# Kernel optimization log

Hardware: AMD Instinct MI355X
Metric: run time of the kernel (lower is better)

The kernel has to match this reference:

```python
import jax, jax.numpy as jnp
import numpy as np

DIM = 1024
H = 16
HD = DIM // H           # head_dim = 64
BS = 64                 # block_size
SPARSITY = 0.95
SCALE = HD ** -0.5


def setup_inputs() -> dict:
    key = jax.random.key(0)
    k1, k2, k3 = jax.random.split(key, 3)
    B, N = 2, 2048
    x = jax.random.normal(k1, (B, N, DIM), jnp.float32)
    # nn.Linear weights (out_features, in_features); qkv has no bias (qkv_bias=False)
    qkv_w = jax.random.normal(k2, (3 * DIM, DIM), jnp.float32) * (DIM ** -0.5)
    proj_w = jax.random.normal(k3, (DIM, DIM), jnp.float32) * (DIM ** -0.5)
    proj_b = jnp.zeros((DIM,), jnp.float32)
    return {"x": x, "qkv_w": qkv_w, "proj_w": proj_w, "proj_b": proj_b}


def reference(x, qkv_w, proj_w, proj_b):
    B, N, D = x.shape
    # qkv projection -> q,k,v each [B,H,N,HD]
    qkv = (x @ qkv_w.T).reshape(B, N, 3, H, HD).transpose(2, 0, 3, 1, 4)
    q, k, v = qkv[0], qkv[1], qkv[2]

    # --- CoarseCurvaturePredictor: block-level affinity + top-k block keep ---
    M = N // BS  # number of blocks (N divisible by block_size here)
    qb = q.reshape(B, H, M, BS, HD).mean(axis=3)  # [B,H,M,HD] coarse queries
    kb = k.reshape(B, H, M, BS, HD).mean(axis=3)  # [B,H,M,HD] coarse keys
    c = jnp.einsum('bhmd,bhnd->bhmn', qb, kb) * SCALE  # block scores [B,H,M,M]
    k_keep = max(1, int(round(M * (1.0 - SPARSITY))))  # blocks kept per row
    thresh = jax.lax.top_k(c, k_keep)[0][..., -1:]
    block_mask = (c >= thresh) | jnp.eye(M, dtype=bool)  # always keep diagonal

    # --- expand block mask to token level (repeat_interleave) ---
    tmask = jnp.repeat(jnp.repeat(block_mask, BS, axis=2), BS, axis=3)  # [B,H,N,N]

    # --- manual dense masked attention (faithful to fallback path) ---
    scores = jnp.einsum('bhqd,bhkd->bhqk', q, k) * SCALE
    scores = jnp.where(tmask, scores, -jnp.inf)
    probs = jax.nn.softmax(scores, axis=-1)
    out = jnp.einsum('bhqk,bhkd->bhqd', probs, v)
    out = out.transpose(0, 2, 1, 3).reshape(B, N, D)
    return out @ proj_w.T + proj_b
```

## Files before the change

kernel.cpp:

```cpp
#include <hip/hip_runtime.h>
#include <hip/hip_bf16.h>

#define BB 2
#define NN 2048
#define DIMD 1024
#define HH 16
#define HD64 64
#define MB 32
#define SCALE_F 0.125f

typedef __attribute__((ext_vector_type(8))) short bf16x8;
typedef __attribute__((ext_vector_type(8))) short short8v;
typedef __attribute__((ext_vector_type(4))) float f32x4;
typedef _Float16 f16;
typedef __attribute__((ext_vector_type(8))) _Float16 f16x8;
typedef __attribute__((ext_vector_type(4))) _Float16 f16x4;

#define VM_WAIT8 asm volatile("s_waitcnt vmcnt(8)" ::: "memory")
#define VM_WAIT6 asm volatile("s_waitcnt vmcnt(6)" ::: "memory")
#define VM_WAIT4 asm volatile("s_waitcnt vmcnt(4)" ::: "memory")
#define VM_WAIT0 asm volatile("s_waitcnt vmcnt(0)" ::: "memory")
#define SBAR __builtin_amdgcn_s_barrier()
#define SCHED0 __builtin_amdgcn_sched_barrier(0)

__device__ __forceinline__ unsigned short bf16_hi(float f) {
    return __builtin_bit_cast(unsigned short, __float2bfloat16(f));
}
__device__ __forceinline__ float bf16_val(unsigned short u) {
    return __bfloat162float(__builtin_bit_cast(__hip_bfloat16, u));
}
__device__ __forceinline__ short f16_bits(float f) {
    return __builtin_bit_cast(short, (f16)f);
}
__device__ __forceinline__ void async_copy16(const void* g, void* l) {
    __builtin_amdgcn_global_load_lds((const __attribute__((address_space(1))) void*)g,
                                     (__attribute__((address_space(3))) void*)l, 16, 0, 0);
}


__global__ __launch_bounds__(256) void split_in_fused_kernel(
    const float* __restrict__ x, short* __restrict__ Axs,
    const float* __restrict__ w, short* __restrict__ Wqs,
    const float* __restrict__ pw, short* __restrict__ Wp)
{
    const int bid = blockIdx.x;
    const float* src; short* dst; int idx;
    if (bid < 4096)      { src = x;  dst = Axs; idx = bid * 256 + threadIdx.x; }
    else if (bid < 7168) { src = w;  dst = Wqs; idx = (bid - 4096) * 256 + threadIdx.x; }
    else                 { src = pw; dst = Wp;  idx = (bid - 7168) * 256 + threadIdx.x; }
    int e = idx * 4;
    float4 v = *(const float4*)(src + e);
    ushort4 o = make_ushort4((unsigned short)f16_bits(v.x), (unsigned short)f16_bits(v.y),
                             (unsigned short)f16_bits(v.z), (unsigned short)f16_bits(v.w));
    *(ushort4*)(dst + e) = o;
}

__global__ __launch_bounds__(256) void qkv_mfma_kernel(
    const short* __restrict__ A, const short* __restrict__ W,
    short* __restrict__ QhI, short* __restrict__ KhI, short* __restrict__ VtI,
    float* __restrict__ qbf, float* __restrict__ kbf)
{
    __shared__ short SM[32768];
    const int wg = blockIdx.x;
    const int row0 = (wg / 24) * 128;
    const int col0 = (wg % 24) * 128;
    const int tid = threadIdx.x;
    const int lane = tid & 63;
    const int wave = tid >> 6;
    const int wm = wave & 1, wn = wave >> 1;

    auto AHS = [&](int b) { return SM + b * 8192; };
    auto WHS = [&](int b) { return SM + 16384 + b * 8192; };

    f32x4 acc[4][4];
    const f32x4 zero = {0.f, 0.f, 0.f, 0.f};
    #pragma unroll
    for (int i = 0; i < 4; ++i)
        #pragma unroll
        for (int j = 0; j < 4; ++j) acc[i][j] = zero;

    const int ldr = lane >> 2;
    const int lko = (((lane & 3) ^ ((lane >> 3) & 3))) * 8;
    const int rsl = ((lane >> 4) ^ ((lane >> 1) & 3)) * 8;

    auto stage = [&](int bufi, int ktn) {
        const int kk = ktn << 6;
        #pragma unroll
        for (int i = 0; i < 2; ++i) {
            const int chunk = wave * 2 + i;
            #pragma unroll
            for (int sub = 0; sub < 2; ++sub) {
                const short* gA = A + (size_t)(row0 + chunk * 16 + ldr) * 1024 + kk + sub * 32 + lko;
                const short* gW = W + (size_t)(col0 + chunk * 16 + ldr) * 1024 + kk + sub * 32 + lko;
                async_copy16(gA, (char*)AHS(bufi) + sub * 8192 + chunk * 1024);
                async_copy16(gW, (char*)WHS(bufi) + sub * 8192 + chunk * 1024);
            }
        }
    };

    auto compute = [&](int bufi) {
        #pragma unroll
        for (int sub = 0; sub < 2; ++sub) {
            const short* Ah = AHS(bufi) + sub * 4096;
            const short* Wh = WHS(bufi) + sub * 4096;
            f16x8 ah[4], wh[4];
            #pragma unroll
            for (int mi = 0; mi < 4; ++mi)
                ah[mi] = *(const f16x8*)(Ah + (wm * 64 + mi * 16 + (lane & 15)) * 32 + rsl);
            #pragma unroll
            for (int ni = 0; ni < 4; ++ni)
                wh[ni] = *(const f16x8*)(Wh + (wn * 64 + ni * 16 + (lane & 15)) * 32 + rsl);
            #pragma unroll
            for (int mi = 0; mi < 4; ++mi)
                #pragma unroll
                for (int ni = 0; ni < 4; ++ni)
                    acc[mi][ni] = __builtin_amdgcn_mfma_f32_16x16x32_f16(ah[mi], wh[ni], acc[mi][ni], 0, 0, 0);
        }
    };

    stage(0, 0);
    for (int kt = 0; kt < 14; kt += 2) {
        stage(1, kt + 1);
        VM_WAIT8; SBAR; SCHED0;
        compute(0);
        SBAR;
        stage(0, kt + 2);
        VM_WAIT8; SBAR; SCHED0;
        compute(1);
        SBAR;
    }
    stage(1, 15);
    VM_WAIT8; SBAR; SCHED0;
    compute(0);
    SBAR;
    VM_WAIT0; SBAR; SCHED0;
    compute(1);
    SBAR;

    const int gr_first = row0 + wm * 64;
    const int bb = gr_first >> 11;
    const int mblk = (gr_first & 2047) >> 6;
    const int gc0 = col0 + wn * 64;
    const int tsel = gc0 >> 10;
    const int h = (gc0 >> 6) & 15;
    const int tile = ((bb << 4) + h) * 32 + mblk;
    const float sc = (tsel == 0) ? SCALE_F : 1.0f;

    if (tsel != 2) {
        short* baseH = ((tsel == 0) ? QhI : KhI) + (size_t)tile * 4096;
        float* mdst  = ((tsel == 0) ? qbf : kbf) + ((size_t)((bb << 4) + h) * 32 + mblk) * 64;
        #pragma unroll
        for (int ni = 0; ni < 4; ++ni) {
            const int d = ni * 16 + (lane & 15);
            float colsum = 0.f;
            #pragma unroll
            for (int mi = 0; mi < 4; ++mi) {
                #pragma unroll
                for (int r = 0; r < 4; ++r) {
                    const int row = mi * 16 + (lane >> 4) * 4 + r;
                    float v = acc[mi][ni][r] * sc;
                    colsum += v;
                    const int off = (row * 64 + d) ^ ((row & 7) << 3);
                    baseH[off] = f16_bits(v);
                }
            }
            colsum += __shfl_xor(colsum, 16);
            colsum += __shfl_xor(colsum, 32);
            if ((lane >> 4) == 0) mdst[d] = colsum * (1.f / 64.f);
        }
    } else {
        short* tb = SM + wave * 4160;
        #pragma unroll
        for (int ni = 0; ni < 4; ++ni)
            #pragma unroll
            for (int mi = 0; mi < 4; ++mi)
                #pragma unroll
                for (int r = 0; r < 4; ++r) {
                    const int row = mi * 16 + (lane >> 4) * 4 + r;
                    const int d = ni * 16 + (lane & 15);
                    tb[row * 65 + d] = f16_bits(acc[mi][ni][r]);
                }
        short* vout = VtI + (size_t)tile * 4096;
        #pragma unroll
        for (int c = 0; c < 8; ++c) {
            short8v tv;
            #pragma unroll
            for (int j = 0; j < 8; ++j)
                tv[j] = tb[(c * 8 + j) * 65 + lane];
            const int off = (lane * 64 + c * 8) ^ ((lane & 7) << 3);
            *(short8v*)(vout + off) = tv;
        }
    }
}

__global__ __launch_bounds__(256) void scores_splitw_kernel(
    const float* __restrict__ qbf, const float* __restrict__ kbf,
    unsigned int* __restrict__ maskbits, float scale,
    const float* __restrict__ projw, short* __restrict__ Wdst)
{
    __shared__ float qs_[32][64];
    __shared__ float ks_[32][64];
    __shared__ float cb[32][32];
    const int bid = blockIdx.x;
    const int tid = threadIdx.x;

    if (bid >= 32) {
        int idx = (bid - 32) * 256 + tid;
        int e = idx * 4;
        float4 v = *(const float4*)(projw + e);
        ushort4 o = make_ushort4((unsigned short)f16_bits(v.x), (unsigned short)f16_bits(v.y),
                                 (unsigned short)f16_bits(v.z), (unsigned short)f16_bits(v.w));
        *(ushort4*)(Wdst + e) = o;
        return;
    }

    #pragma unroll
    for (int i = 0; i < 8; ++i) {
        int e = tid + i * 256;
        qs_[e >> 6][e & 63] = qbf[(size_t)bid * 2048 + e];
        ks_[e >> 6][e & 63] = kbf[(size_t)bid * 2048 + e];
    }
    __syncthreads();

    #pragma unroll
    for (int i = 0; i < 4; ++i) {
        int idx = tid + i * 256;
        int r = idx >> 5, c = idx & 31;
        float s = 0.f;
        #pragma unroll
        for (int d = 0; d < 64; ++d) s += qs_[r][d] * ks_[c][d];
        cb[r][c] = s * scale;
    }
    __syncthreads();

    if (tid < 32) {
        float m1 = -INFINITY, m2 = -INFINITY;
        for (int n = 0; n < 32; ++n) {
            float v = cb[tid][n];
            if (v > m1) { m2 = m1; m1 = v; }
            else if (v > m2) { m2 = v; }
        }
        unsigned int bits = 1u << tid;
        for (int n = 0; n < 32; ++n)
            if (cb[tid][n] >= m2) bits |= 1u << n;
        maskbits[bid * 32 + tid] = bits;
    }
}

__global__ __launch_bounds__(256) void proj_mfma_kernel(
    const short* __restrict__ A, const short* __restrict__ W,
    const float* __restrict__ bias, float* __restrict__ out)
{
    __shared__ short Ahs[2][8192];
    __shared__ short Whs[2][4096];
    const int bid = blockIdx.x;
    const int wg = (bid & 7) * 64 + (bid >> 3);
    const int row0 = (wg >> 4) * 128;
    const int col0 = (wg & 15) * 64;
    const int tid = threadIdx.x;
    const int lane = tid & 63;
    const int wave = tid >> 6;

    f32x4 acc[2][4];
    const f32x4 zero = {0.f, 0.f, 0.f, 0.f};
    #pragma unroll
    for (int i = 0; i < 2; ++i)
        #pragma unroll
        for (int j = 0; j < 4; ++j) acc[i][j] = zero;

    const int ldr = lane >> 2;
    const int lko = (((lane & 3) ^ ((lane >> 3) & 3))) * 8;
    const int rsl = ((lane >> 4) ^ ((lane >> 1) & 3)) * 8;

    auto stage = [&](int bufi, int ktn) {
        const int kk = ktn << 6;
        #pragma unroll
        for (int i = 0; i < 2; ++i) {
            const int chunk = wave * 2 + i;
            #pragma unroll
            for (int sub = 0; sub < 2; ++sub) {
                const short* gA = A + (size_t)(row0 + chunk * 16 + ldr) * 1024 + kk + sub * 32 + lko;
                async_copy16(gA, (char*)&Ahs[bufi][0] + sub * 8192 + chunk * 1024);
            }
        }
        #pragma unroll
        for (int sub = 0; sub < 2; ++sub) {
            const short* gW = W + (size_t)(col0 + wave * 16 + ldr) * 1024 + kk + sub * 32 + lko;
            async_copy16(gW, (char*)&Whs[bufi][0] + sub * 4096 + wave * 1024);
        }
    };

    auto compute = [&](int bufi) {
        #pragma unroll
        for (int sub = 0; sub < 2; ++sub) {
            const short* Ah = &Ahs[bufi][0] + sub * 4096;
            const short* Wh = &Whs[bufi][0] + sub * 2048;
            f16x8 ah[2], wh[4];
            #pragma unroll
            for (int mi = 0; mi < 2; ++mi)
                ah[mi] = *(const f16x8*)(Ah + (wave * 32 + mi * 16 + (lane & 15)) * 32 + rsl);
            #pragma unroll
            for (int ni = 0; ni < 4; ++ni)
                wh[ni] = *(const f16x8*)(Wh + (ni * 16 + (lane & 15)) * 32 + rsl);
            #pragma unroll
            for (int mi = 0; mi < 2; ++mi)
                #pragma unroll
                for (int ni = 0; ni < 4; ++ni)
                    acc[mi][ni] = __builtin_amdgcn_mfma_f32_16x16x32_f16(ah[mi], wh[ni], acc[mi][ni], 0, 0, 0);
        }
    };

    stage(0, 0);
    for (int kt = 0; kt < 14; kt += 2) {
        stage(1, kt + 1);
        VM_WAIT6; SBAR; SCHED0;
        compute(0);
        SBAR;
        stage(0, kt + 2);
        VM_WAIT6; SBAR; SCHED0;
        compute(1);
        SBAR;
    }
    stage(1, 15);
    VM_WAIT6; SBAR; SCHED0;
    compute(0);
    SBAR;
    VM_WAIT0; SBAR; SCHED0;
    compute(1);

    #pragma unroll
    for (int ni = 0; ni < 4; ++ni) {
        int gc = col0 + ni * 16 + (lane & 15);
        float bv = bias[gc];
        #pragma unroll
        for (int mi = 0; mi < 2; ++mi) {
            int gr0 = row0 + wave * 32 + mi * 16 + (lane >> 4) * 4;
            #pragma unroll
            for (int r = 0; r < 4; ++r)
                out[(size_t)(gr0 + r) * 1024 + gc] = acc[mi][ni][r] + bv;
        }
    }
}

__global__ __launch_bounds__(256) void sparse_attn_mfma_kernel(
    const short* __restrict__ QhI, const short* __restrict__ KhI,
    const short* __restrict__ VtI,
    const float* __restrict__ qbf, const float* __restrict__ kbf,
    short* __restrict__ aout)
{
    __shared__ f16 Kh[2][4096];
    __shared__ f16 Vt[2][4096];
    __shared__ f16 Pb[4096];

    const int bid = blockIdx.x;
    const int wg = (bid & 7) * 128 + (bid >> 3);
    const int m  = wg & 31;
    const int bh = wg >> 5;
    const int b  = bh >> 4, h = bh & 15;
    const int tid = threadIdx.x;
    const int lane = tid & 63;
    const int wave = tid >> 6;
    const f32x4 zero = {0.f, 0.f, 0.f, 0.f};

    const int arow = wave * 16 + (lane & 15);
    const int kofs = (lane >> 4) * 8;
    const int colb = (lane >> 4) * 16;
    const int pswz = (arow & 7) << 3;

    auto stageKV = [&](int bufi, int nb) {
        const size_t t4 = (size_t)(bh * 32 + nb) * 4096;
        const int so = wave * 1024 + lane * 8;
        async_copy16(KhI + t4 + so,       (char*)&Kh[bufi][0] + wave * 2048);
        async_copy16(KhI + t4 + so + 512, (char*)&Kh[bufi][0] + wave * 2048 + 1024);
        async_copy16(VtI + t4 + so,       (char*)&Vt[bufi][0] + wave * 2048);
        async_copy16(VtI + t4 + so + 512, (char*)&Vt[bufi][0] + wave * 2048 + 1024);
    };

    stageKV(0, m);

    f16x8 qreg[2];
    {
        const short* qt = QhI + (size_t)(bh * 32 + m) * 4096;
        #pragma unroll
        for (int c = 0; c < 2; ++c) {
            const int qoff = (arow * 128 + c * 64 + colb) ^ ((arow & 7) << 4);
            qreg[c] = *(const f16x8*)((const char*)qt + qoff);
        }
    }

    unsigned int mask;
    {
        float c = -INFINITY;
        if (lane < 32) {
            const float* qrow = qbf + ((size_t)bh * 32 + m) * 64;
            const float* krow = kbf + ((size_t)bh * 32 + lane) * 64;
            float s = 0.f;
            for (int d = 0; d < 64; ++d) s += qrow[d] * krow[d];
            c = s;
        }
        float m1 = c;
        #pragma unroll
        for (int off = 1; off < 64; off <<= 1) m1 = fmaxf(m1, __shfl_xor(m1, off));
        unsigned long long eq = __ballot(c == m1);
        float cx = (c == m1) ? -INFINITY : c;
        #pragma unroll
        for (int off = 1; off < 64; off <<= 1) cx = fmaxf(cx, __shfl_xor(cx, off));
        float m2 = (__popcll(eq) >= 2) ? m1 : cx;
        unsigned long long ge = __ballot(c >= m2);
        mask = (unsigned int)(ge & 0xffffffffULL) | (1u << m);
    }

    f32x4 o_acc[4];
    float macc_s = -INFINITY, lacc_s = 0.f;
    #pragma unroll
    for (int t = 0; t < 4; ++t) o_acc[t] = zero;

    auto computeTile = [&](int bi) {
        const f16* KhB = &Kh[bi][0];
        f32x4 s_acc[4];
        #pragma unroll
        for (int t = 0; t < 4; ++t) s_acc[t] = zero;
        #pragma unroll
        for (int c = 0; c < 2; ++c) {
            #pragma unroll
            for (int t = 0; t < 4; ++t) {
                const int krow = t * 16 + (lane & 15);
                const int koff = (krow * 128 + c * 64 + colb) ^ ((krow & 7) << 4);
                f16x8 bh_ = *(const f16x8*)((const char*)KhB + koff);
                s_acc[t] = __builtin_amdgcn_mfma_f32_16x16x32_f16(bh_, qreg[c], s_acc[t], 0, 0, 0);
            }
        }

        float vmax = s_acc[0][0];
        #pragma unroll
        for (int t = 0; t < 4; ++t)
            #pragma unroll
            for (int r = 0; r < 4; ++r) vmax = fmaxf(vmax, s_acc[t][r]);
        vmax = fmaxf(vmax, __shfl_xor(vmax, 16));
        vmax = fmaxf(vmax, __shfl_xor(vmax, 32));
        float mnew = fmaxf(macc_s, vmax);
        float alpha = expf(macc_s - mnew);
        macc_s = mnew;

        float psum = 0.f;
        #pragma unroll
        for (int t = 0; t < 4; ++t) {
            f16x4 pv;
            #pragma unroll
            for (int r = 0; r < 4; ++r) {
                float p = expf(s_acc[t][r] - mnew);
                psum += p;
                pv[r] = (f16)p;
            }
            *(f16x4*)(Pb + ((arow * 64 + t * 16 + (lane >> 4) * 4) ^ pswz)) = pv;
        }
        psum += __shfl_xor(psum, 16);
        psum += __shfl_xor(psum, 32);
        lacc_s = lacc_s * alpha + psum;

        float ab[4];
        #pragma unroll
        for (int r = 0; r < 4; ++r) ab[r] = __shfl(alpha, (lane >> 4) * 4 + r);
        #pragma unroll
        for (int t = 0; t < 4; ++t)
            #pragma unroll
            for (int r = 0; r < 4; ++r) o_acc[t][r] *= ab[r];

        const f16* VtB = &Vt[bi][0];
        #pragma unroll
        for (int c = 0; c < 2; ++c) {
            f16x8 af = *(const f16x8*)(Pb + ((arow * 64 + c * 32 + kofs) ^ pswz));
            #pragma unroll
            for (int t = 0; t < 4; ++t) {
                const int vrow = t * 16 + (lane & 15);
                const int voff = (vrow * 128 + c * 64 + colb) ^ ((vrow & 7) << 4);
                f16x8 bf = *(const f16x8*)((const char*)VtB + voff);
                o_acc[t] = __builtin_amdgcn_mfma_f32_16x16x32_f16(af, bf, o_acc[t], 0, 0, 0);
            }
        }
    };

    unsigned int mm = mask & ~(1u << m);
    int cur = 0;
    for (;;) {
        int nb_nxt = -1;
        if (mm) { nb_nxt = __builtin_ctz(mm); mm &= mm - 1; stageKV(cur ^ 1, nb_nxt); }
        if (nb_nxt >= 0) { VM_WAIT4; } else { VM_WAIT0; }
        SBAR; SCHED0;
        computeTile(cur);
        SBAR;
        if (nb_nxt < 0) break;
        cur ^= 1;
    }

    float inv_s = (lacc_s > 0.f) ? (1.f / lacc_s) : 0.f;
    float invb[4];
    #pragma unroll
    for (int r = 0; r < 4; ++r) invb[r] = __shfl(inv_s, (lane >> 4) * 4 + r);
    #pragma unroll
    for (int t = 0; t < 4; ++t) {
        int gc = h * 64 + t * 16 + (lane & 15);
        #pragma unroll
        for (int r = 0; r < 4; ++r) {
            int grow = b * NN + m * 64 + wave * 16 + (lane >> 4) * 4 + r;
            float v = o_acc[t][r] * invb[r];
            aout[(size_t)grow * 1024 + gc] = f16_bits(v);
        }
    }
}


__global__ __launch_bounds__(256) void block_mean_kernel(
    const float* __restrict__ qf, const float* __restrict__ kf,
    float* __restrict__ qbf, float* __restrict__ kbf)
{
    int idx = blockIdx.x * 256 + threadIdx.x;
    const float* src = (idx < 65536) ? qf : kf;
    float* dst       = (idx < 65536) ? qbf : kbf;
    int e = idx & 65535;
    int d = e & 63;
    int r = e >> 6;
    size_t base = (size_t)r * 4096 + d;
    float s = 0.f;
    #pragma unroll
    for (int i = 0; i < 64; ++i) s += src[base + (size_t)i * 64];
    dst[e] = s * (1.f / 64.f);
}

__global__ __launch_bounds__(256) void qkv_gemm_fb(
    const float* __restrict__ x, const float* __restrict__ w,
    float* __restrict__ qf, float* __restrict__ kf, float* __restrict__ vf)
{
    __shared__ float As[64][33];
    __shared__ float Bs[64][33];
    const int tid = threadIdx.x;
    const int row0 = blockIdx.y * 64;
    const int col0 = blockIdx.x * 64;
    const int ty = tid >> 4, tx = tid & 15;

    float acc[4][4] = {};
    for (int k0 = 0; k0 < 1024; k0 += 32) {
        #pragma unroll
        for (int i = 0; i < 8; ++i) {
            int e = tid + i * 256;
            int r = e >> 5, c = e & 31;
            As[r][c] = x[(size_t)(row0 + r) * 1024 + k0 + c];
            Bs[r][c] = w[(size_t)(col0 + r) * 1024 + k0 + c];
        }
        __syncthreads();
        #pragma unroll
        for (int kk = 0; kk < 32; ++kk) {
            float a[4], bq[4];
            #pragma unroll
            for (int i = 0; i < 4; ++i) a[i] = As[ty * 4 + i][kk];
            #pragma unroll
            for (int j = 0; j < 4; ++j) bq[j] = Bs[tx * 4 + j][kk];
            #pragma unroll
            for (int i = 0; i < 4; ++i)
                #pragma unroll
                for (int j = 0; j < 4; ++j)
                    acc[i][j] += a[i] * bq[j];
        }
        __syncthreads();
    }

    const int tsel = col0 >> 10;
    const int h    = (col0 & 1023) >> 6;
    float* dstbuf = (tsel == 0) ? qf : (tsel == 1) ? kf : vf;
    #pragma unroll
    for (int i = 0; i < 4; ++i) {
        int row = row0 + ty * 4 + i;
        int b   = row >> 11, n = row & 2047;
        size_t rb = ((size_t)(b * HH + h) * NN + n) * HD64;
        #pragma unroll
        for (int j = 0; j < 4; ++j)
            dstbuf[rb + tx * 4 + j] = acc[i][j];
    }
}

__global__ __launch_bounds__(256) void proj_gemm_fb(
    const float* __restrict__ attn, const float* __restrict__ w,
    const float* __restrict__ bias, float* __restrict__ out)
{
    __shared__ float As[64][33];
    __shared__ float Bs[64][33];
    const int tid = threadIdx.x;
    const int row0 = blockIdx.y * 64;
    const int col0 = blockIdx.x * 64;
    const int ty = tid >> 4, tx = tid & 15;

    float acc[4][4] = {};
    for (int k0 = 0; k0 < 1024; k0 += 32) {
        #pragma unroll
        for (int i = 0; i < 8; ++i) {
            int e = tid + i * 256;
            int r = e >> 5, c = e & 31;
            As[r][c] = attn[(size_t)(row0 + r) * 1024 + k0 + c];
            Bs[r][c] = w[(size_t)(col0 + r) * 1024 + k0 + c];
        }
        __syncthreads();
        #pragma unroll
        for (int kk = 0; kk < 32; ++kk) {
            float a[4], bq[4];
            #pragma unroll
            for (int i = 0; i < 4; ++i) a[i] = As[ty * 4 + i][kk];
            #pragma unroll
            for (int j = 0; j < 4; ++j) bq[j] = Bs[tx * 4 + j][kk];
            #pragma unroll
            for (int i = 0; i < 4; ++i)
                #pragma unroll
                for (int j = 0; j < 4; ++j)
                    acc[i][j] += a[i] * bq[j];
        }
        __syncthreads();
    }

    #pragma unroll
    for (int j = 0; j < 4; ++j) {
        int col = col0 + tx * 4 + j;
        float bv = bias[col];
        #pragma unroll
        for (int i = 0; i < 4; ++i) {
            int row = row0 + ty * 4 + i;
            out[(size_t)row * 1024 + col] = acc[i][j] + bv;
        }
    }
}

__global__ __launch_bounds__(256) void sparse_attn_fb(
    const float* __restrict__ qf, const float* __restrict__ kf,
    const float* __restrict__ vf, const unsigned int* __restrict__ maskbits,
    float* __restrict__ attnf)
{
    __shared__ float kbuf[64][64];
    __shared__ float vbuf[64][64];
    __shared__ float sbuf[64][65];
    const int m  = blockIdx.x & 31;
    const int bh = blockIdx.x >> 5;
    const int b  = bh >> 4, h = bh & 15;
    const int t  = threadIdx.x;
    const int qr = t >> 2;
    const int dg = t & 3;
    const int d0 = dg * 16;

    float qreg[16];
    {
        const float* qp = qf + ((size_t)bh * NN + m * 64 + qr) * HD64 + d0;
        #pragma unroll
        for (int j = 0; j < 16; j += 4) {
            float4 v = *(const float4*)(qp + j);
            qreg[j] = v.x; qreg[j+1] = v.y; qreg[j+2] = v.z; qreg[j+3] = v.w;
        }
    }

    const unsigned int mask = maskbits[bh * 32 + m];
    float macc = -INFINITY, lacc = 0.f;
    float oacc[16];
    #pragma unroll
    for (int j = 0; j < 16; ++j) oacc[j] = 0.f;

    for (int nb = 0; nb < 32; ++nb) {
        if (!((mask >> nb) & 1u)) continue;
        __syncthreads();
        {
            const float* gk = kf + ((size_t)bh * NN + nb * 64) * HD64;
            const float* gv = vf + ((size_t)bh * NN + nb * 64) * HD64;
            #pragma unroll
            for (int i = 0; i < 4; ++i) {
                async_copy16(gk + t * 4 + i * 1024, (char*)kbuf + t * 16 + i * 4096);
                async_copy16(gv + t * 4 + i * 1024, (char*)vbuf + t * 16 + i * 4096);
            }
        }
        __syncthreads();

        float bmax = -INFINITY;
        for (int kk = 0; kk < 64; ++kk) {
            float s = 0.f;
            #pragma unroll
            for (int j = 0; j < 16; ++j) s += qreg[j] * kbuf[kk][d0 + j];
            s += __shfl_xor(s, 1);
            s += __shfl_xor(s, 2);
            s *= SCALE_F;
            if (dg == 0) sbuf[qr][kk] = s;
            bmax = fmaxf(bmax, s);
        }
        float mnew  = fmaxf(macc, bmax);
        float alpha = expf(macc - mnew);
        lacc *= alpha;
        #pragma unroll
        for (int j = 0; j < 16; ++j) oacc[j] *= alpha;
        for (int kk = 0; kk < 64; ++kk) {
            float p = expf(sbuf[qr][kk] - mnew);
            lacc += p;
            #pragma unroll
            for (int j = 0; j < 16; ++j) oacc[j] += p * vbuf[kk][d0 + j];
        }
        macc = mnew;
    }

    float inv = (lacc > 0.f) ? (1.f / lacc) : 0.f;
    size_t orow = ((size_t)(b * NN + m * 64 + qr)) * DIMD + h * 64 + d0;
    #pragma unroll
    for (int j = 0; j < 16; ++j) attnf[orow + j] = oacc[j] * inv;
}

extern "C" void kernel_launch(void* const* d_in, const int* in_sizes, int n_in,
                              void* d_out, int out_size, void* d_ws, size_t ws_size,
                              hipStream_t stream)
{
    const float* x      = (const float*)d_in[0];
    const float* qkv_w  = (const float*)d_in[1];
    const float* proj_w = (const float*)d_in[2];
    const float* proj_b = (const float*)d_in[3];
    float* out = (float*)d_out;

    short* QhI = (short*)d_ws;
    short* KhI = QhI + 4194304;
    short* VtI = KhI + 4194304;
    float* qbf = (float*)(VtI + 4194304);
    float* kbf = qbf + 65536;
    unsigned int* maskb = (unsigned int*)(kbf + 65536);
    short* Axs = (short*)(maskb + 1024);
    short* Wqs = Axs + (size_t)4096 * 1024;
    short* Wp  = Wqs + (size_t)3072 * 1024;
    const size_t need_fast = (size_t)((char*)(Wp + (size_t)1024 * 1024) - (char*)d_ws);

    if (ws_size >= need_fast) {
        split_in_fused_kernel<<<8192, 256, 0, stream>>>(x, Axs, qkv_w, Wqs, proj_w, Wp);
        qkv_mfma_kernel<<<768, 256, 0, stream>>>(Axs, Wqs, QhI, KhI, VtI, qbf, kbf);
        sparse_attn_mfma_kernel<<<1024, 256, 0, stream>>>(QhI, KhI, VtI, qbf, kbf, Axs);
        proj_mfma_kernel<<<512, 256, 0, stream>>>(Axs, Wp, proj_b, out);
    } else {
        float* qf2  = (float*)d_ws;
        float* kf2  = qf2 + 4194304;
        float* vf2  = kf2 + 4194304;
        float* qbf2 = vf2 + 4194304;
        float* kbf2 = qbf2 + 65536;
        unsigned int* maskb2 = (unsigned int*)(kbf2 + 65536);
        float* attnf = (float*)(maskb2 + 1024);
        qkv_gemm_fb<<<dim3(48, 64), 256, 0, stream>>>(x, qkv_w, qf2, kf2, vf2);
        block_mean_kernel<<<512, 256, 0, stream>>>(qf2, kf2, qbf2, kbf2);
        scores_splitw_kernel<<<32, 256, 0, stream>>>(qbf2, kbf2, maskb2, SCALE_F,
                                                     (const float*)nullptr, (short*)nullptr);
        sparse_attn_fb<<<1024, 256, 0, stream>>>(qf2, kf2, vf2, maskb2, attnf);
        proj_gemm_fb<<<dim3(16, 64), 256, 0, stream>>>(attnf, proj_w, proj_b, out);
    }
}
```

Before: 147.7 us.

## Read K/V tiles directly from global memory instead of LDS double-buffering

Removes the async global-to-LDS double-buffered staging of K and V tiles, along with its waitcnt and barrier synchronisation. Each wave now loads its MFMA fragments straight from global memory through the same swizzled offsets. With only a few kept blocks per query row, this is meant to cut staging overhead and barriers and to free LDS for higher occupancy. The cost is that all four waves fetch the same K/V data separately through the cache, and global-load latency is no longer hidden by prefetching.

```diff
diff --git a/kernel.cpp b/kernel.cpp
--- a/kernel.cpp
+++ b/kernel.cpp
@@ -18,7 +18,6 @@
 
 #define VM_WAIT8 asm volatile("s_waitcnt vmcnt(8)" ::: "memory")
 #define VM_WAIT6 asm volatile("s_waitcnt vmcnt(6)" ::: "memory")
-#define VM_WAIT4 asm volatile("s_waitcnt vmcnt(4)" ::: "memory")
 #define VM_WAIT0 asm volatile("s_waitcnt vmcnt(0)" ::: "memory")
 #define SBAR __builtin_amdgcn_s_barrier()
 #define SCHED0 __builtin_amdgcn_sched_barrier(0)
@@ -348,8 +347,6 @@
     const float* __restrict__ qbf, const float* __restrict__ kbf,
     short* __restrict__ aout)
 {
-    __shared__ f16 Kh[2][4096];
-    __shared__ f16 Vt[2][4096];
     __shared__ f16 Pb[4096];
 
     const int bid = blockIdx.x;
@@ -367,17 +364,6 @@
     const int colb = (lane >> 4) * 16;
     const int pswz = (arow & 7) << 3;
 
-    auto stageKV = [&](int bufi, int nb) {
-        const size_t t4 = (size_t)(bh * 32 + nb) * 4096;
-        const int so = wave * 1024 + lane * 8;
-        async_copy16(KhI + t4 + so,       (char*)&Kh[bufi][0] + wave * 2048);
-        async_copy16(KhI + t4 + so + 512, (char*)&Kh[bufi][0] + wave * 2048 + 1024);
-        async_copy16(VtI + t4 + so,       (char*)&Vt[bufi][0] + wave * 2048);
-        async_copy16(VtI + t4 + so + 512, (char*)&Vt[bufi][0] + wave * 2048 + 1024);
-    };
-
-    stageKV(0, m);
-
     f16x8 qreg[2];
     {
         const short* qt = QhI + (size_t)(bh * 32 + m) * 4096;
@@ -415,8 +401,10 @@
     #pragma unroll
     for (int t = 0; t < 4; ++t) o_acc[t] = zero;
 
-    auto computeTile = [&](int bi) {
-        const f16* KhB = &Kh[bi][0];
+    auto computeTile = [&](int nb) {
+        const size_t t4 = (size_t)(bh * 32 + nb) * 4096;
+        const char* KhB = (const char*)(KhI + t4);
+        const char* VtB = (const char*)(VtI + t4);
         f32x4 s_acc[4];
         #pragma unroll
         for (int t = 0; t < 4; ++t) s_acc[t] = zero;
@@ -426,7 +414,7 @@
             for (int t = 0; t < 4; ++t) {
                 const int krow = t * 16 + (lane & 15);
                 const int koff = (krow * 128 + c * 64 + colb) ^ ((krow & 7) << 4);
-                f16x8 bh_ = *(const f16x8*)((const char*)KhB + koff);
+                f16x8 bh_ = *(const f16x8*)(KhB + koff);
                 s_acc[t] = __builtin_amdgcn_mfma_f32_16x16x32_f16(bh_, qreg[c], s_acc[t], 0, 0, 0);
             }
         }
@@ -466,7 +454,6 @@
             #pragma unroll
             for (int r = 0; r < 4; ++r) o_acc[t][r] *= ab[r];
 
-        const f16* VtB = &Vt[bi][0];
         #pragma unroll
         for (int c = 0; c < 2; ++c) {
             f16x8 af = *(const f16x8*)(Pb + ((arow * 64 + c * 32 + kofs) ^ pswz));
@@ -474,23 +461,17 @@
             for (int t = 0; t < 4; ++t) {
                 const int vrow = t * 16 + (lane & 15);
                 const int voff = (vrow * 128 + c * 64 + colb) ^ ((vrow & 7) << 4);
-                f16x8 bf = *(const f16x8*)((const char*)VtB + voff);
+                f16x8 bf = *(const f16x8*)(VtB + voff);
                 o_acc[t] = __builtin_amdgcn_mfma_f32_16x16x32_f16(af, bf, o_acc[t], 0, 0, 0);
             }
         }
     };
 
+    computeTile(m);
     unsigned int mm = mask & ~(1u << m);
-    int cur = 0;
-    for (;;) {
-        int nb_nxt = -1;
-        if (mm) { nb_nxt = __builtin_ctz(mm); mm &= mm - 1; stageKV(cur ^ 1, nb_nxt); }
-        if (nb_nxt >= 0) { VM_WAIT4; } else { VM_WAIT0; }
-        SBAR; SCHED0;
-        computeTile(cur);
-        SBAR;
-        if (nb_nxt < 0) break;
-        cur ^= 1;
+    while (mm) {
+        int nb = __builtin_ctz(mm); mm &= mm - 1;
+        computeTile(nb);
     }
 
     float inv_s = (lacc_s > 0.f) ? (1.f / lacc_s) : 0.f;
```

Measured after the change: 151.5 us. +2.6%, slower.
